# Kernel tuning notes

Measured on AMD Instinct MI355X. Metric: run time of the kernel, lower is better.

Reference implementation:

```python
import jax, jax.numpy as jnp
import numpy as np

S_LEN, B, H, V, L = 128, 128, 1024, 32000, 2
H2 = 512  # ceil(H/2)
WSZ = 10
MAXW = 2 * WSZ + 1


def setup_inputs() -> dict:
    key = jax.random.key(0)
    k = jax.random.split(key, 16)
    def n(ki, shape, s=0.02):
        return jax.random.normal(ki, shape, dtype=jnp.float32) * s
    return {
        "source_sentence_length": S_LEN,
        "encoder_output": jax.random.normal(k[0], (S_LEN, B, H), dtype=jnp.float32),
        "word": jax.random.randint(k[1], (1, B), 0, V),
        "h0": jax.random.normal(k[2], (L, B, H), dtype=jnp.float32),
        "c0": jax.random.normal(k[3], (L, B, H), dtype=jnp.float32),
        "embedding": n(k[4], (V, H)),
        "lstm_Wih": n(k[5], (L, 4 * H, H)),
        "lstm_Whh": n(k[6], (L, 4 * H, H)),
        "lstm_bih": jnp.zeros((L, 4 * H), jnp.float32),
        "lstm_bhh": jnp.zeros((L, 4 * H), jnp.float32),
        "attn_w1": n(k[7], (H2, H)),
        "attn_b1": jnp.zeros((H2,), jnp.float32),
        "attn_w2": n(k[8], (1, H2)),
        "attn_b2": jnp.zeros((1,), jnp.float32),
        "fc1_w": n(k[9], (H, 2 * H)),
        "fc1_b": jnp.zeros((H,), jnp.float32),
        "fc2_w": n(k[10], (V, H)),
        "fc2_b": jnp.zeros((V,), jnp.float32),
    }


def reference(source_sentence_length, encoder_output, word, h0, c0, embedding,
              lstm_Wih, lstm_Whh, lstm_bih, lstm_bhh,
              attn_w1, attn_b1, attn_w2, attn_b2,
              fc1_w, fc1_b, fc2_w, fc2_b):
    S = source_sentence_length
    std2 = (WSZ / 2.0) ** 2  # std_squared from the module

    # embedding lookup: word [1,B] -> [1,B,H]; single-step multi-layer LSTM
    x = embedding[word][0]  # [B,H]
    hs, cs = [], []
    for l in range(h0.shape[0]):
        gates = x @ lstm_Wih[l].T + lstm_bih[l] + h0[l] @ lstm_Whh[l].T + lstm_bhh[l]
        i, f, g, o = jnp.split(gates, 4, axis=-1)
        c = jax.nn.sigmoid(f) * c0[l] + jax.nn.sigmoid(i) * jnp.tanh(g)
        h = jax.nn.sigmoid(o) * jnp.tanh(c)
        hs.append(h); cs.append(c); x = h
    h_new = jnp.stack(hs)
    c_new = jnp.stack(cs)
    out = x[None]  # decoder output [1,B,H]

    # predicted window center p in [0,S]
    p = S * jax.nn.sigmoid(jnp.tanh(out @ attn_w1.T + attn_b1) @ attn_w2.T + attn_b2)
    pb = p[0, :, 0]  # [B]
    ws = jnp.round(jnp.clip(pb - WSZ, 0, None)).astype(jnp.int32)
    we = jnp.round(jnp.clip(pb + WSZ, None, S - 1)).astype(jnp.int32)

    # windowed gather: position j of window b is source index ws[b]+j
    idx = ws[:, None] + jnp.arange(MAXW, dtype=jnp.int32)  # [B,MAXW]
    valid = idx <= we[:, None]
    enc_b = encoder_output.transpose(1, 0, 2)  # [B,S,H]
    h_s = jnp.take_along_axis(enc_b, jnp.clip(idx, 0, S - 1)[:, :, None], axis=1)
    h_s = jnp.where(valid[:, :, None], h_s, 0.0)  # zero-padded as in the torch code

    # faithful (non-negative, non-squared) gaussian term: exp((pos - p)/(2*std^2))
    gauss = jnp.where(valid, jnp.exp((idx.astype(enc_b.dtype) - pb[:, None]) / (2.0 * std2)), 0.0)

    scores = jnp.einsum('bh,bwh->bw', out[0], h_s)  # zero-padded slots score 0, kept in softmax
    a = jax.nn.softmax(scores, axis=-1) * gauss  # [B,MAXW]
    ctx = jnp.einsum('bw,bwh->bh', a, h_s)[None]  # [1,B,H]

    cat = jnp.concatenate([ctx, out], axis=2)  # [1,B,2H]
    o2 = jnp.tanh(cat @ fc1_w.T + fc1_b)
    y = jax.nn.log_softmax(o2 @ fc2_w.T + fc2_b, axis=2)  # [1,B,V]
    return (y, o2, h_new, c_new, a)
```

## Files before the change

kernel.cpp:

```cpp
#include <hip/hip_runtime.h>
#include <math.h>

namespace {

constexpr int B    = 128;
constexpr int H    = 1024;
constexpr int V    = 32000;
constexpr int WSZ  = 10;
constexpr int MAXW = 2 * WSZ + 1;

typedef __attribute__((ext_vector_type(8))) short bf16x8;
typedef __attribute__((ext_vector_type(4))) short short4v;
typedef __attribute__((ext_vector_type(4))) float f32x4;

__device__ __forceinline__ float sigf(float x) { return 1.0f / (1.0f + expf(-x)); }

__device__ __forceinline__ unsigned short rnebf(float f) {
    unsigned u = __float_as_uint(f);
    u += 0x7fffu + ((u >> 16) & 1u);
    return (unsigned short)(u >> 16);
}

__device__ __forceinline__ bf16x8 cvt8(const f32x4 a, const f32x4 b) {
    bf16x8 r;
    r[0] = (short)rnebf(a.x); r[1] = (short)rnebf(a.y);
    r[2] = (short)rnebf(a.z); r[3] = (short)rnebf(a.w);
    r[4] = (short)rnebf(b.x); r[5] = (short)rnebf(b.y);
    r[6] = (short)rnebf(b.z); r[7] = (short)rnebf(b.w);
    return r;
}

__device__ __forceinline__ void gl_lds16(const float* g, float* l) {
    __builtin_amdgcn_global_load_lds(
        (const __attribute__((address_space(1))) unsigned int*)g,
        (__attribute__((address_space(3))) unsigned int*)l,
        16, 0, 0);
}

struct S3 { short h, m, l; };

__device__ __forceinline__ S3 split3(float x) {
    S3 r;
    const unsigned uh = __float_as_uint(x) & 0xFFFF0000u;
    const float fh = __uint_as_float(uh);
    const float r1 = x - fh;
    const unsigned um = __float_as_uint(r1) & 0xFFFF0000u;
    const float fm = __uint_as_float(um);
    const float r2 = r1 - fm;
    const unsigned ul = __float_as_uint(r2) & 0xFFFF0000u;
    r.h = (short)(uh >> 16);
    r.m = (short)(um >> 16);
    r.l = (short)(ul >> 16);
    return r;
}

__device__ __forceinline__ void split8(const f32x4 a, const f32x4 b,
                                       bf16x8& wh, bf16x8& wm, bf16x8& wl) {
    S3 s;
    s = split3(a.x); wh[0] = s.h; wm[0] = s.m; wl[0] = s.l;
    s = split3(a.y); wh[1] = s.h; wm[1] = s.m; wl[1] = s.l;
    s = split3(a.z); wh[2] = s.h; wm[2] = s.m; wl[2] = s.l;
    s = split3(a.w); wh[3] = s.h; wm[3] = s.m; wl[3] = s.l;
    s = split3(b.x); wh[4] = s.h; wm[4] = s.m; wl[4] = s.l;
    s = split3(b.y); wh[5] = s.h; wm[5] = s.m; wl[5] = s.l;
    s = split3(b.z); wh[6] = s.h; wm[6] = s.m; wl[6] = s.l;
    s = split3(b.w); wh[7] = s.h; wm[7] = s.m; wl[7] = s.l;
}

__global__ __launch_bounds__(256, 2) void lstm_gemm(
    const short* __restrict__ Ah0, const short* __restrict__ Am0, const short* __restrict__ Al0,
    const short* __restrict__ Ah1, const short* __restrict__ Am1, const short* __restrict__ Al1,
    const float* __restrict__ W0, const float* __restrict__ W1,
    float* __restrict__ outbase)
{
    __shared__ float wt[2][4160];

    const int t    = threadIdx.x;
    const int lane = t & 63;
    const int w    = t >> 6;
    const int m16  = lane & 15;
    const int g    = lane >> 4;
    const int n0   = blockIdx.x * 64;
    const int y    = blockIdx.y;
    const int src  = y >> 2;
    const int k0   = (y & 3) * 256;
    const short* Ah = src ? Ah1 : Ah0;
    const short* Am = src ? Am1 : Am0;
    const short* Al = src ? Al1 : Al0;
    const float* W  = src ? W1  : W0;
    float* out = outbase + (size_t)y * 128 * 4096;

    bf16x8 ah[2][8], am[2][8], al[2][8];
    #pragma unroll
    for (int q = 0; q < 2; ++q) {
        const size_t ao = (size_t)((w * 2 + q) * 16 + m16) * 1024 + k0 + g * 8;
        #pragma unroll
        for (int s = 0; s < 8; ++s) {
            ah[q][s] = *(const bf16x8*)(Ah + ao + s * 32);
            am[q][s] = *(const bf16x8*)(Am + ao + s * 32);
            al[q][s] = *(const bf16x8*)(Al + ao + s * 32);
        }
    }

#define LSTM_STAGE(BUF, C)                                                  \
    {                                                                       \
        _Pragma("unroll")                                                   \
        for (int i = 0; i < 5; ++i) {                                       \
            const int idx = i * 256 + t;                                    \
            const int rr  = idx / 65;                                       \
            const int pp  = idx - rr * 65;                                  \
            if (idx < 1040 && pp < 64) {                                    \
                const float* s_ = W + (size_t)(n0 + (C) * 16 + rr) * 1024   \
                                + k0 + pp * 4;                              \
                gl_lds16(s_, &wt[BUF][(size_t)(i * 256 + w * 64) * 4]);     \
            }                                                               \
        }                                                                   \
    }

    LSTM_STAGE(0, 0)
    int cur = 0;
    #pragma unroll
    for (int c = 0; c < 4; ++c) {
        __syncthreads();
        if (c < 3) {
            if (cur == 0) LSTM_STAGE(1, c + 1)
            else          LSTM_STAGE(0, c + 1)
        }
        f32x4 acc0 = {}, acc1 = {};
        const float* lrow = &wt[cur][m16 * 260 + g * 8];
        #pragma unroll
        for (int s = 0; s < 8; ++s) {
            const f32x4 wa = *(const f32x4*)(lrow + s * 32);
            const f32x4 wb = *(const f32x4*)(lrow + s * 32 + 4);
            bf16x8 wh, wm, wl;
            split8(wa, wb, wh, wm, wl);
            acc0 = __builtin_amdgcn_mfma_f32_16x16x32_bf16(ah[0][s], wh, acc0, 0, 0, 0);
            acc0 = __builtin_amdgcn_mfma_f32_16x16x32_bf16(ah[0][s], wm, acc0, 0, 0, 0);
            acc0 = __builtin_amdgcn_mfma_f32_16x16x32_bf16(am[0][s], wh, acc0, 0, 0, 0);
            acc0 = __builtin_amdgcn_mfma_f32_16x16x32_bf16(ah[0][s], wl, acc0, 0, 0, 0);
            acc0 = __builtin_amdgcn_mfma_f32_16x16x32_bf16(am[0][s], wm, acc0, 0, 0, 0);
            acc0 = __builtin_amdgcn_mfma_f32_16x16x32_bf16(al[0][s], wh, acc0, 0, 0, 0);
            acc1 = __builtin_amdgcn_mfma_f32_16x16x32_bf16(ah[1][s], wh, acc1, 0, 0, 0);
            acc1 = __builtin_amdgcn_mfma_f32_16x16x32_bf16(ah[1][s], wm, acc1, 0, 0, 0);
            acc1 = __builtin_amdgcn_mfma_f32_16x16x32_bf16(am[1][s], wh, acc1, 0, 0, 0);
            acc1 = __builtin_amdgcn_mfma_f32_16x16x32_bf16(ah[1][s], wl, acc1, 0, 0, 0);
            acc1 = __builtin_amdgcn_mfma_f32_16x16x32_bf16(am[1][s], wm, acc1, 0, 0, 0);
            acc1 = __builtin_amdgcn_mfma_f32_16x16x32_bf16(al[1][s], wh, acc1, 0, 0, 0);
        }
        const int col = n0 + c * 16 + m16;
        #pragma unroll
        for (int j = 0; j < 4; ++j) {
            out[(size_t)(w * 32 + g * 4 + j) * 4096 + col]      = acc0[j];
            out[(size_t)(w * 32 + 16 + g * 4 + j) * 4096 + col] = acc1[j];
        }
        cur ^= 1;
    }
#undef LSTM_STAGE
}

__global__ __launch_bounds__(256, 2) void fc2_gemm(
    const short* __restrict__ A, const float* __restrict__ W,
    const float* __restrict__ bias, float* __restrict__ out)
{
    __shared__ float wt[2][16 * 516];

    const int t    = threadIdx.x;
    const int lane = t & 63;
    const int w    = t >> 6;
    const int m16  = lane & 15;
    const int g    = lane >> 4;
    const int n0   = blockIdx.x * 64;

    bf16x8 a[2][32];
    #pragma unroll
    for (int q = 0; q < 2; ++q) {
        const short* ap = A + (size_t)((w * 2 + q) * 16 + m16) * 1024 + g * 8;
        #pragma unroll
        for (int s = 0; s < 32; ++s)
            a[q][s] = *(const bf16x8*)(ap + s * 32);
    }

#define FC2_STAGE(BUF, C)                                                   \
    {                                                                       \
        _Pragma("unroll")                                                   \
        for (int i = 0; i < 9; ++i) {                                       \
            const int idx = i * 256 + t;                                    \
            const int rr  = idx / 129;                                      \
            const int pp  = idx - rr * 129;                                 \
            if (idx < 2064 && pp < 128) {                                   \
                const float* src = W                                        \
                    + (size_t)(n0 + ((C) >> 1) * 16 + rr) * 1024            \
                    + ((C) & 1) * 512 + pp * 4;                             \
                gl_lds16(src, &wt[BUF][(size_t)(i * 256 + w * 64) * 4]);    \
            }                                                               \
        }                                                                   \
    }

    FC2_STAGE(0, 0)
    int cur = 0;
    f32x4 acc0 = {}, acc1 = {};
    #pragma unroll
    for (int c = 0; c < 8; ++c) {
        __syncthreads();
        if (c < 7) {
            if (cur == 0) FC2_STAGE(1, c + 1)
            else          FC2_STAGE(0, c + 1)
        }
        if ((c & 1) == 0) { acc0 = {}; acc1 = {}; }
        const float* lrow = &wt[cur][m16 * 516 + g * 8];
        #pragma unroll
        for (int s = 0; s < 16; ++s) {
            const f32x4 wa = *(const f32x4*)(lrow + s * 32);
            const f32x4 wb = *(const f32x4*)(lrow + s * 32 + 4);
            const bf16x8 bfr = cvt8(wa, wb);
            const int ks = (c & 1) * 16 + s;
            acc0 = __builtin_amdgcn_mfma_f32_16x16x32_bf16(a[0][ks], bfr, acc0, 0, 0, 0);
            acc1 = __builtin_amdgcn_mfma_f32_16x16x32_bf16(a[1][ks], bfr, acc1, 0, 0, 0);
        }
        if (c & 1) {
            const int col = n0 + (c >> 1) * 16 + m16;
            const float bv = bias[col];
            #pragma unroll
            for (int j = 0; j < 4; ++j) {
                out[(size_t)(w * 32 + g * 4 + j) * V + col]      = acc0[j] + bv;
                out[(size_t)(w * 32 + 16 + g * 4 + j) * V + col] = acc1[j] + bv;
            }
        }
        cur ^= 1;
    }
#undef FC2_STAGE
}

__global__ __launch_bounds__(256, 2) void gemm_x3(
    const short* __restrict__ Ah0, const short* __restrict__ Am0, const short* __restrict__ Al0,
    const short* __restrict__ Ah1, const short* __restrict__ Am1, const short* __restrict__ Al1,
    const float* __restrict__ W0, const float* __restrict__ W1,
    int N, int Ksz, int ks_log2, float* __restrict__ outbase)
{
    const int y = blockIdx.y;
    const int src = y >> ks_log2;
    const short* Ah = src ? Ah1 : Ah0;
    const short* Am = src ? Am1 : Am0;
    const short* Al = src ? Al1 : Al0;
    const float* W  = src ? W1  : W0;
    const int k0 = (y & ((1 << ks_log2) - 1)) * Ksz;
    float* out = outbase + (size_t)y * 128 * N;

    const int t    = threadIdx.x;
    const int lane = t & 63;
    const int wv   = t >> 6;
    const int n0   = blockIdx.x * 64 + wv * 16;
    const int m16  = lane & 15;
    const int ko8  = (lane >> 4) * 8;

    const float* wp = W + (size_t)(n0 + m16) * 1024 + k0 + ko8;
    const size_t a0 = (size_t)m16 * 1024 + k0 + ko8;

    f32x4 acc[8] = {};

    f32x4 cwa = *(const f32x4*)(wp);      f32x4 cwb = *(const f32x4*)(wp + 4);
    f32x4 nwa = *(const f32x4*)(wp + 32); f32x4 nwb = *(const f32x4*)(wp + 36);

    for (int kc = 0; kc + 64 < Ksz; kc += 32) {
        bf16x8 ah[8], am[8], al[8];
        #pragma unroll
        for (int m = 0; m < 8; ++m) {
            const size_t ao = a0 + (size_t)m * 16384 + kc;
            ah[m] = *(const bf16x8*)(Ah + ao);
            am[m] = *(const bf16x8*)(Am + ao);
            al[m] = *(const bf16x8*)(Al + ao);
        }
        __builtin_amdgcn_sched_barrier(0);
        const f32x4 fwa = *(const f32x4*)(wp + kc + 64);
        const f32x4 fwb = *(const f32x4*)(wp + kc + 68);
        bf16x8 wh, wm, wl;
        split8(cwa, cwb, wh, wm, wl);
        #pragma unroll
        for (int m = 0; m < 8; ++m) {
            acc[m] = __builtin_amdgcn_mfma_f32_16x16x32_bf16(ah[m], wh, acc[m], 0, 0, 0);
            acc[m] = __builtin_amdgcn_mfma_f32_16x16x32_bf16(ah[m], wm, acc[m], 0, 0, 0);
            acc[m] = __builtin_amdgcn_mfma_f32_16x16x32_bf16(am[m], wh, acc[m], 0, 0, 0);
            acc[m] = __builtin_amdgcn_mfma_f32_16x16x32_bf16(ah[m], wl, acc[m], 0, 0, 0);
            acc[m] = __builtin_amdgcn_mfma_f32_16x16x32_bf16(am[m], wm, acc[m], 0, 0, 0);
            acc[m] = __builtin_amdgcn_mfma_f32_16x16x32_bf16(al[m], wh, acc[m], 0, 0, 0);
        }
        cwa = nwa; cwb = nwb; nwa = fwa; nwb = fwb;
    }
    #pragma unroll
    for (int tail = 0; tail < 2; ++tail) {
        const int kc = Ksz - 64 + tail * 32;
        bf16x8 ah[8], am[8], al[8];
        #pragma unroll
        for (int m = 0; m < 8; ++m) {
            const size_t ao = a0 + (size_t)m * 16384 + kc;
            ah[m] = *(const bf16x8*)(Ah + ao);
            am[m] = *(const bf16x8*)(Am + ao);
            al[m] = *(const bf16x8*)(Al + ao);
        }
        const f32x4 wa = tail ? nwa : cwa;
        const f32x4 wb = tail ? nwb : cwb;
        bf16x8 wh, wm, wl;
        split8(wa, wb, wh, wm, wl);
        #pragma unroll
        for (int m = 0; m < 8; ++m) {
            acc[m] = __builtin_amdgcn_mfma_f32_16x16x32_bf16(ah[m], wh, acc[m], 0, 0, 0);
            acc[m] = __builtin_amdgcn_mfma_f32_16x16x32_bf16(ah[m], wm, acc[m], 0, 0, 0);
            acc[m] = __builtin_amdgcn_mfma_f32_16x16x32_bf16(am[m], wh, acc[m], 0, 0, 0);
            acc[m] = __builtin_amdgcn_mfma_f32_16x16x32_bf16(ah[m], wl, acc[m], 0, 0, 0);
            acc[m] = __builtin_amdgcn_mfma_f32_16x16x32_bf16(am[m], wm, acc[m], 0, 0, 0);
            acc[m] = __builtin_amdgcn_mfma_f32_16x16x32_bf16(al[m], wh, acc[m], 0, 0, 0);
        }
    }

    #pragma unroll
    for (int m = 0; m < 8; ++m) {
        const int rbase = m * 16 + (lane >> 4) * 4;
        #pragma unroll
        for (int r = 0; r < 4; ++r)
            out[(size_t)(rbase + r) * N + n0 + m16] = acc[m][r];
    }
}

__global__ __launch_bounds__(256, 2) void fc1_gemm(
    const short* __restrict__ A0, const short* __restrict__ A1,
    const float* __restrict__ W, float* __restrict__ outbase)
{
    __shared__ float wt[2][16 * 132];

    const int t    = threadIdx.x;
    const int lane = t & 63;
    const int w    = t >> 6;
    const int m16  = lane & 15;
    const int g    = lane >> 4;
    const int n0   = blockIdx.x * 64;
    const int y    = blockIdx.y;
    const int src  = y >> 3;
    const int k0   = (y & 7) * 128;
    const int wk0  = src * 1024 + k0;
    const short* A = src ? A1 : A0;
    float* out = outbase + (size_t)y * 128 * 1024;

    bf16x8 a[2][4];
    #pragma unroll
    for (int q = 0; q < 2; ++q) {
        const short* ap = A + (size_t)((w * 2 + q) * 16 + m16) * 1024 + k0 + g * 8;
        #pragma unroll
        for (int s = 0; s < 4; ++s)
            a[q][s] = *(const bf16x8*)(ap + s * 32);
    }

#define FC1_STAGE(BUF, C)                                                   \
    {                                                                       \
        _Pragma("unroll")                                                   \
        for (int i = 0; i < 3; ++i) {                                       \
            const int idx = i * 256 + t;                                    \
            const int rr  = idx / 33;                                       \
            const int pp  = idx - rr * 33;                                  \
            if (idx < 528 && pp < 32) {                                     \
                const float* s_ = W + (size_t)(n0 + (C) * 16 + rr) * 2048   \
                                + wk0 + pp * 4;                             \
                gl_lds16(s_, &wt[BUF][(size_t)(i * 256 + w * 64) * 4]);     \
            }                                                               \
        }                                                                   \
    }

    FC1_STAGE(0, 0)
    int cur = 0;
    #pragma unroll
    for (int c = 0; c < 4; ++c) {
        __syncthreads();
        if (c < 3) {
            if (cur == 0) FC1_STAGE(1, c + 1)
            else          FC1_STAGE(0, c + 1)
        }
        f32x4 acc0 = {}, acc1 = {};
        const float* lrow = &wt[cur][m16 * 132 + g * 8];
        #pragma unroll
        for (int s = 0; s < 4; ++s) {
            const f32x4 wa = *(const f32x4*)(lrow + s * 32);
            const f32x4 wb = *(const f32x4*)(lrow + s * 32 + 4);
            const bf16x8 bfr = cvt8(wa, wb);
            acc0 = __builtin_amdgcn_mfma_f32_16x16x32_bf16(a[0][s], bfr, acc0, 0, 0, 0);
            acc1 = __builtin_amdgcn_mfma_f32_16x16x32_bf16(a[1][s], bfr, acc1, 0, 0, 0);
        }
        const int col = n0 + c * 16 + m16;
        #pragma unroll
        for (int j = 0; j < 4; ++j) {
            out[(size_t)(w * 32 + g * 4 + j) * 1024 + col]      = acc0[j];
            out[(size_t)(w * 32 + 16 + g * 4 + j) * 1024 + col] = acc1[j];
        }
        cur ^= 1;
    }
#undef FC1_STAGE
}

__global__ void prep_k(const int* __restrict__ word, const float* __restrict__ emb,
                       const float* __restrict__ h0,
                       short* __restrict__ xh, short* __restrict__ xm, short* __restrict__ xl,
                       short* __restrict__ h0h, short* __restrict__ h0m, short* __restrict__ h0l)
{
    const int blk = blockIdx.x, t = threadIdx.x;
    const float* src; short *dh, *dm, *dl; size_t off;
    if (blk < 128) {
        src = emb + (size_t)word[blk] * H; off = (size_t)blk * H;
        dh = xh; dm = xm; dl = xl;
    } else {
        const int i = blk - 128;
        src = h0 + (size_t)i * H; off = (size_t)i * H;
        dh = h0h; dm = h0m; dl = h0l;
    }
    const float4 v = ((const float4*)src)[t];
    short4v sh, sm, sl;
    S3 s;
    s = split3(v.x); sh.x = s.h; sm.x = s.m; sl.x = s.l;
    s = split3(v.y); sh.y = s.h; sm.y = s.m; sl.y = s.l;
    s = split3(v.z); sh.z = s.h; sm.z = s.m; sl.z = s.l;
    s = split3(v.w); sh.w = s.h; sm.w = s.m; sl.w = s.l;
    *(short4v*)(dh + off + t * 4) = sh;
    *(short4v*)(dm + off + t * 4) = sm;
    *(short4v*)(dl + off + t * 4) = sl;
}

__global__ void lstm_cell_k(const float* __restrict__ part,
                            const float* __restrict__ bih, const float* __restrict__ bhh,
                            const float* __restrict__ c0,
                            float* __restrict__ h_out, float* __restrict__ c_out,
                            short* __restrict__ xh, short* __restrict__ xm,
                            short* __restrict__ xl)
{
    const int idx = blockIdx.x * 256 + threadIdx.x;
    const int b = idx >> 10, hh = idx & 1023;
    const size_t base = (size_t)b * 4096;
    float g[4];
    #pragma unroll
    for (int j = 0; j < 4; ++j) {
        const int o = hh + j * H;
        float s = bih[o] + bhh[o];
        #pragma unroll
        for (int i = 0; i < 8; ++i) s += part[base + o + (size_t)i * 524288];
        g[j] = s;
    }
    const float c = sigf(g[1]) * c0[idx] + sigf(g[0]) * tanhf(g[2]);
    const float h = sigf(g[3]) * tanhf(c);
    c_out[idx] = c;
    h_out[idx] = h;
    const S3 s = split3(h);
    xh[idx] = s.h; xm[idx] = s.m; xl[idx] = s.l;
}

__global__ void attn_ctx_k(const float* __restrict__ part, const float* __restrict__ b1,
                           const float* __restrict__ w2v, const float* __restrict__ b2,
                           const int* __restrict__ Sptr,
                           const float* __restrict__ x, const float* __restrict__ enc,
                           float* __restrict__ a_out, short* __restrict__ ctxb)
{
    __shared__ float red[256];
    __shared__ float so[H];
    __shared__ float swred[4][MAXW];
    __shared__ float ssc[MAXW];
    __shared__ float sa[MAXW];
    __shared__ float sp;
    __shared__ int sw0, sw1;
    const int b = blockIdx.x, t = threadIdx.x;
    const int lane = t & 63, wvv = t >> 6;

    {
        const float* pa = part + (size_t)b * 512;
        float v = 0.f;
        #pragma unroll
        for (int jj = 0; jj < 2; ++jj) {
            const int j = t + jj * 256;
            float sgm = b1[j];
            #pragma unroll
            for (int i = 0; i < 16; ++i) sgm += pa[j + (size_t)i * 65536];
            v += tanhf(sgm) * w2v[j];
        }
        red[t] = v;
        __syncthreads();
        for (int s = 128; s > 0; s >>= 1) {
            if (t < s) red[t] += red[t + s];
            __syncthreads();
        }
        if (t == 0) {
            const float S = (float)Sptr[0];
            const float sv = S * sigf(red[0] + b2[0]);
            sp  = sv;
            sw0 = (int)rintf(fmaxf(sv - (float)WSZ, 0.f));
            sw1 = (int)rintf(fminf(sv + (float)WSZ, S - 1.f));
        }
    }
    for (int h = t; h < H; h += 256) so[h] = x[(size_t)b * H + h];
    __syncthreads();
    const int w0 = sw0, w1e = sw1;
    const float pbv = sp;

    float ps[MAXW];
    #pragma unroll
    for (int w = 0; w < MAXW; ++w) ps[w] = 0.f;
    for (int h4 = t; h4 < H / 4; h4 += 256) {
        const float4 o = ((const float4*)so)[h4];
        #pragma unroll
        for (int w = 0; w < MAXW; ++w) {
            const int idx = w0 + w;
            if (idx <= w1e) {
                const float4 e = *(const float4*)(enc + ((size_t)idx * B + b) * H + h4 * 4);
                ps[w] += o.x * e.x + o.y * e.y + o.z * e.z + o.w * e.w;
            }
        }
    }
    #pragma unroll
    for (int w = 0; w < MAXW; ++w) {
        float v = ps[w];
        for (int off = 32; off > 0; off >>= 1) v += __shfl_down(v, off);
        if (lane == 0) swred[wvv][w] = v;
    }
    __syncthreads();
    if (t == 0) {
        float m = -1e30f;
        for (int w = 0; w < MAXW; ++w) {
            const float s = swred[0][w] + swred[1][w] + swred[2][w] + swred[3][w];
            ssc[w] = s;
            m = fmaxf(m, s);
        }
        float den = 0.f;
        for (int w = 0; w < MAXW; ++w) den += expf(ssc[w] - m);
        for (int w = 0; w < MAXW; ++w) {
            const int idx = w0 + w;
            const float gauss = (idx <= w1e) ? expf(((float)idx - pbv) / 50.0f) : 0.f;
            sa[w] = expf(ssc[w] - m) / den * gauss;
        }
    }
    __syncthreads();
    if (t < MAXW) a_out[b * MAXW + t] = sa[t];
    for (int h4 = t; h4 < H / 4; h4 += 256) {
        float4 acc = {0.f, 0.f, 0.f, 0.f};
        #pragma unroll
        for (int w = 0; w < MAXW; ++w) {
            const int idx = w0 + w;
            if (idx <= w1e) {
                const float4 e = *(const float4*)(enc + ((size_t)idx * B + b) * H + h4 * 4);
                acc.x += sa[w] * e.x; acc.y += sa[w] * e.y;
                acc.z += sa[w] * e.z; acc.w += sa[w] * e.w;
            }
        }
        short4v s;
        s.x = (short)rnebf(acc.x); s.y = (short)rnebf(acc.y);
        s.z = (short)rnebf(acc.z); s.w = (short)rnebf(acc.w);
        *(short4v*)(ctxb + (size_t)b * H + h4 * 4) = s;
    }
}

__global__ void fc1_fin_k(const float* __restrict__ part, const float* __restrict__ bias,
                          float* __restrict__ o2, short* __restrict__ o2b)
{
    const int idx = blockIdx.x * 256 + threadIdx.x;
    const int n = idx & 1023;
    float v = bias[n];
    #pragma unroll
    for (int i = 0; i < 16; ++i) v += part[idx + (size_t)i * 131072];
    v = tanhf(v);
    o2[idx] = v;
    o2b[idx] = (short)rnebf(v);
}

__global__ __launch_bounds__(1024) void lsm_k(float* __restrict__ y)
{
    __shared__ float sm[16], ss[16], slse;
    const int b = blockIdx.x, t = threadIdx.x;
    float* yrow = y + (size_t)b * V;

    f32x4 r[8];
    float m = -1e30f, s = 0.f;
    #pragma unroll
    for (int i = 0; i < 8; ++i) {
        const int v4 = t + i * 1024;
        if (v4 < V / 4) {
            const f32x4 q = ((const f32x4*)yrow)[v4];
            r[i] = q;
            const float mm = fmaxf(fmaxf(q.x, q.y), fmaxf(q.z, q.w));
            if (mm > m) { s *= expf(m - mm); m = mm; }
            s += expf(q.x - m) + expf(q.y - m) + expf(q.z - m) + expf(q.w - m);
        }
    }
    for (int off = 32; off > 0; off >>= 1) {
        const float mo = __shfl_down(m, off), so = __shfl_down(s, off);
        const float mn = fmaxf(m, mo);
        s = s * expf(m - mn) + so * expf(mo - mn);
        m = mn;
    }
    const int wv = t >> 6, lane = t & 63;
    if (lane == 0) { sm[wv] = m; ss[wv] = s; }
    __syncthreads();
    if (t == 0) {
        float M = sm[0], S = ss[0];
        for (int i = 1; i < 16; ++i) {
            const float mn = fmaxf(M, sm[i]);
            S = S * expf(M - mn) + ss[i] * expf(sm[i] - mn);
            M = mn;
        }
        slse = M + logf(S);
    }
    __syncthreads();
    const float lse = slse;
    #pragma unroll
    for (int i = 0; i < 8; ++i) {
        const int v4 = t + i * 1024;
        if (v4 < V / 4) {
            f32x4 q = r[i];
            q.x -= lse; q.y -= lse; q.z -= lse; q.w -= lse;
            ((f32x4*)yrow)[v4] = q;
        }
    }
}

}

extern "C" void kernel_launch(void* const* d_in, const int* in_sizes, int n_in,
                              void* d_out, int out_size, void* d_ws, size_t ws_size,
                              hipStream_t stream)
{
    const int*   Sp   = (const int*)d_in[0];
    const float* enc  = (const float*)d_in[1];
    const int*   word = (const int*)d_in[2];
    const float* h0   = (const float*)d_in[3];
    const float* c0   = (const float*)d_in[4];
    const float* emb  = (const float*)d_in[5];
    const float* Wih  = (const float*)d_in[6];
    const float* Whh  = (const float*)d_in[7];
    const float* bih  = (const float*)d_in[8];
    const float* bhh  = (const float*)d_in[9];
    const float* aw1  = (const float*)d_in[10];
    const float* ab1  = (const float*)d_in[11];
    const float* aw2  = (const float*)d_in[12];
    const float* ab2  = (const float*)d_in[13];
    const float* f1w  = (const float*)d_in[14];
    const float* f1b  = (const float*)d_in[15];
    const float* f2w  = (const float*)d_in[16];
    const float* f2b  = (const float*)d_in[17];

    float* outp = (float*)d_out;
    float* y    = outp;
    float* o2   = y  + (size_t)B * V;
    float* hN   = o2 + (size_t)B * H;
    float* cN   = hN + 2 * (size_t)B * H;
    float* aO   = cN + 2 * (size_t)B * H;

    char* wsp = (char*)d_ws;
    short* xh   = (short*)wsp;  wsp += (size_t)B * H * 2;
    short* xm   = (short*)wsp;  wsp += (size_t)B * H * 2;
    short* xl   = (short*)wsp;  wsp += (size_t)B * H * 2;
    short* h0h  = (short*)wsp;  wsp += (size_t)2 * B * H * 2;
    short* h0m  = (short*)wsp;  wsp += (size_t)2 * B * H * 2;
    short* h0l  = (short*)wsp;  wsp += (size_t)2 * B * H * 2;
    short* ctxb = (short*)wsp;  wsp += (size_t)B * H * 2;
    short* o2b  = (short*)wsp;  wsp += (size_t)B * H * 2;
    float* part = (float*)wsp;  wsp += (size_t)16 * B * 4 * H * 4;

    prep_k<<<dim3(384), dim3(256), 0, stream>>>(word, emb, h0, xh, xm, xl, h0h, h0m, h0l);

    for (int l = 0; l < 2; ++l) {
        lstm_gemm<<<dim3(64, 8), dim3(256), 0, stream>>>(
            xh, xm, xl,
            h0h + (size_t)l * B * H, h0m + (size_t)l * B * H, h0l + (size_t)l * B * H,
            Wih + (size_t)l * 4 * H * H, Whh + (size_t)l * 4 * H * H,
            part);
        lstm_cell_k<<<dim3(B * H / 256), dim3(256), 0, stream>>>(
            part, bih + (size_t)l * 4 * H, bhh + (size_t)l * 4 * H,
            c0 + (size_t)l * B * H,
            hN + (size_t)l * B * H, cN + (size_t)l * B * H, xh, xm, xl);
    }

    const float* hfin = hN + (size_t)B * H;

    gemm_x3<<<dim3(8, 16), dim3(256), 0, stream>>>(
        xh, xm, xl, xh, xm, xl, aw1, aw1, 512, 64, 4, part);
    attn_ctx_k<<<dim3(B), dim3(256), 0, stream>>>(
        part, ab1, aw2, ab2, Sp, hfin, enc, aO, ctxb);

    fc1_gemm<<<dim3(16, 16), dim3(256), 0, stream>>>(ctxb, xh, f1w, part);
    fc1_fin_k<<<dim3(B * H / 256), dim3(256), 0, stream>>>(part, f1b, o2, o2b);

    fc2_gemm<<<dim3(V / 64), dim3(256), 0, stream>>>(o2b, f2w, f2b, y);

    lsm_k<<<dim3(B), dim3(1024), 0, stream>>>(y);
}
```

Measured before the change: 200.5 us.

## Split fc2 GEMM along K into two partials and fold sum plus bias into log-softmax

The fc2 GEMM now runs as a 500x2 grid, each block covering half of K (512), and writes float partial logits to a new workspace buffer. The log-softmax kernel reads both partials plus the bias and sums them before reducing, so the bias add leaves the GEMM epilogue. The K split doubles the block count and halves A-fragment registers per thread, and the 2-blocks-per-CU launch bound is dropped. In exchange an extra B*V*4 bytes of partial output is written and read back, adding memory traffic.

```diff
diff --git a/kernel.cpp b/kernel.cpp
--- a/kernel.cpp
+++ b/kernel.cpp
@@ -158,9 +158,9 @@
 #undef LSTM_STAGE
 }
 
-__global__ __launch_bounds__(256, 2) void fc2_gemm(
+__global__ __launch_bounds__(256) void fc2_gemm(
     const short* __restrict__ A, const float* __restrict__ W,
-    const float* __restrict__ bias, float* __restrict__ out)
+    float* __restrict__ outbase)
 {
     __shared__ float wt[2][16 * 516];
 
@@ -170,13 +170,16 @@
     const int m16  = lane & 15;
     const int g    = lane >> 4;
     const int n0   = blockIdx.x * 64;
-
-    bf16x8 a[2][32];
+    const int y    = blockIdx.y;
+    const int k0   = y * 512;
+    float* out = outbase + (size_t)y * B * V;
+
+    bf16x8 a[2][16];
     #pragma unroll
     for (int q = 0; q < 2; ++q) {
-        const short* ap = A + (size_t)((w * 2 + q) * 16 + m16) * 1024 + g * 8;
-        #pragma unroll
-        for (int s = 0; s < 32; ++s)
+        const short* ap = A + (size_t)((w * 2 + q) * 16 + m16) * 1024 + k0 + g * 8;
+        #pragma unroll
+        for (int s = 0; s < 16; ++s)
             a[q][s] = *(const bf16x8*)(ap + s * 32);
     }
 
@@ -188,9 +191,8 @@
             const int rr  = idx / 129;                                      \
             const int pp  = idx - rr * 129;                                 \
             if (idx < 2064 && pp < 128) {                                   \
-                const float* src = W                                        \
-                    + (size_t)(n0 + ((C) >> 1) * 16 + rr) * 1024            \
-                    + ((C) & 1) * 512 + pp * 4;                             \
+                const float* src = W + (size_t)(n0 + (C) * 16 + rr) * 1024  \
+                                 + k0 + pp * 4;                             \
                 gl_lds16(src, &wt[BUF][(size_t)(i * 256 + w * 64) * 4]);    \
             }                                                               \
         }                                                                   \
@@ -198,33 +200,28 @@
 
     FC2_STAGE(0, 0)
     int cur = 0;
-    f32x4 acc0 = {}, acc1 = {};
-    #pragma unroll
-    for (int c = 0; c < 8; ++c) {
+    #pragma unroll
+    for (int c = 0; c < 4; ++c) {
         __syncthreads();
-        if (c < 7) {
+        if (c < 3) {
             if (cur == 0) FC2_STAGE(1, c + 1)
             else          FC2_STAGE(0, c + 1)
         }
-        if ((c & 1) == 0) { acc0 = {}; acc1 = {}; }
+        f32x4 acc0 = {}, acc1 = {};
         const float* lrow = &wt[cur][m16 * 516 + g * 8];
         #pragma unroll
         for (int s = 0; s < 16; ++s) {
             const f32x4 wa = *(const f32x4*)(lrow + s * 32);
             const f32x4 wb = *(const f32x4*)(lrow + s * 32 + 4);
             const bf16x8 bfr = cvt8(wa, wb);
-            const int ks = (c & 1) * 16 + s;
-            acc0 = __builtin_amdgcn_mfma_f32_16x16x32_bf16(a[0][ks], bfr, acc0, 0, 0, 0);
-            acc1 = __builtin_amdgcn_mfma_f32_16x16x32_bf16(a[1][ks], bfr, acc1, 0, 0, 0);
-        }
-        if (c & 1) {
-            const int col = n0 + (c >> 1) * 16 + m16;
-            const float bv = bias[col];
-            #pragma unroll
-            for (int j = 0; j < 4; ++j) {
-                out[(size_t)(w * 32 + g * 4 + j) * V + col]      = acc0[j] + bv;
-                out[(size_t)(w * 32 + 16 + g * 4 + j) * V + col] = acc1[j] + bv;
-            }
+            acc0 = __builtin_amdgcn_mfma_f32_16x16x32_bf16(a[0][s], bfr, acc0, 0, 0, 0);
+            acc1 = __builtin_amdgcn_mfma_f32_16x16x32_bf16(a[1][s], bfr, acc1, 0, 0, 0);
+        }
+        const int col = n0 + c * 16 + m16;
+        #pragma unroll
+        for (int j = 0; j < 4; ++j) {
+            out[(size_t)(w * 32 + g * 4 + j) * V + col]      = acc0[j];
+            out[(size_t)(w * 32 + 16 + g * 4 + j) * V + col] = acc1[j];
         }
         cur ^= 1;
     }
@@ -563,10 +560,14 @@
     o2b[idx] = (short)rnebf(v);
 }
 
-__global__ __launch_bounds__(1024) void lsm_k(float* __restrict__ y)
+__global__ __launch_bounds__(1024) void lsm_k(
+    const float* __restrict__ p0, const float* __restrict__ p1,
+    const float* __restrict__ bias, float* __restrict__ y)
 {
     __shared__ float sm[16], ss[16], slse;
     const int b = blockIdx.x, t = threadIdx.x;
+    const float* r0 = p0 + (size_t)b * V;
+    const float* r1 = p1 + (size_t)b * V;
     float* yrow = y + (size_t)b * V;
 
     f32x4 r[8];
@@ -575,7 +576,12 @@
     for (int i = 0; i < 8; ++i) {
         const int v4 = t + i * 1024;
         if (v4 < V / 4) {
-            const f32x4 q = ((const f32x4*)yrow)[v4];
+            const f32x4 a = ((const f32x4*)r0)[v4];
+            const f32x4 c = ((const f32x4*)r1)[v4];
+            const f32x4 bv = ((const f32x4*)bias)[v4];
+            f32x4 q;
+            q.x = a.x + c.x + bv.x; q.y = a.y + c.y + bv.y;
+            q.z = a.z + c.z + bv.z; q.w = a.w + c.w + bv.w;
             r[i] = q;
             const float mm = fmaxf(fmaxf(q.x, q.y), fmaxf(q.z, q.w));
             if (mm > m) { s *= expf(m - mm); m = mm; }
@@ -655,6 +661,7 @@
     short* ctxb = (short*)wsp;  wsp += (size_t)B * H * 2;
     short* o2b  = (short*)wsp;  wsp += (size_t)B * H * 2;
     float* part = (float*)wsp;  wsp += (size_t)16 * B * 4 * H * 4;
+    float* pf2  = (float*)wsp;  wsp += (size_t)2 * B * V * 4;
 
     prep_k<<<dim3(384), dim3(256), 0, stream>>>(word, emb, h0, xh, xm, xl, h0h, h0m, h0l);
 
@@ -680,7 +687,7 @@
     fc1_gemm<<<dim3(16, 16), dim3(256), 0, stream>>>(ctxb, xh, f1w, part);
     fc1_fin_k<<<dim3(B * H / 256), dim3(256), 0, stream>>>(part, f1b, o2, o2b);
 
-    fc2_gemm<<<dim3(V / 64), dim3(256), 0, stream>>>(o2b, f2w, f2b, y);
-
-    lsm_k<<<dim3(B), dim3(1024), 0, stream>>>(y);
-}
+    fc2_gemm<<<dim3(V / 64, 2), dim3(256), 0, stream>>>(o2b, f2w, pf2);
+
+    lsm_k<<<dim3(B), dim3(1024), 0, stream>>>(pf2, pf2 + (size_t)B * V, f2b, y);
+}
```

Result: faster. 168.8 us (median of 2 runs) (-15.8%).

## Reorder fc2 GEMM loop to load A in K-halves with persistent accumulators

Applied to the files above, without the earlier changes.

The fc2 GEMM now walks the K dimension in two halves. Each wave loads only half of its A fragments (16 per row tile instead of 32) and accumulates all four 16-column output tiles in registers, writing them out at the end. This cuts the live A register footprint, which is meant to reduce register pressure or spills. It also drops the launch_bounds minimum-blocks hint. In exchange it holds 8 accumulators and reloads A once per K-half, and occupancy may change.

```diff
diff --git a/kernel.cpp b/kernel.cpp
--- a/kernel.cpp
+++ b/kernel.cpp
@@ -158,7 +158,7 @@
 #undef LSTM_STAGE
 }
 
-__global__ __launch_bounds__(256, 2) void fc2_gemm(
+__global__ __launch_bounds__(256) void fc2_gemm(
     const short* __restrict__ A, const float* __restrict__ W,
     const float* __restrict__ bias, float* __restrict__ out)
 {
@@ -171,16 +171,9 @@
     const int g    = lane >> 4;
     const int n0   = blockIdx.x * 64;
 
-    bf16x8 a[2][32];
-    #pragma unroll
-    for (int q = 0; q < 2; ++q) {
-        const short* ap = A + (size_t)((w * 2 + q) * 16 + m16) * 1024 + g * 8;
-        #pragma unroll
-        for (int s = 0; s < 32; ++s)
-            a[q][s] = *(const bf16x8*)(ap + s * 32);
-    }
-
-#define FC2_STAGE(BUF, C)                                                   \
+    f32x4 acc[4][2] = {};
+
+#define FC2_STAGE(BUF, KH, C)                                               \
     {                                                                       \
         _Pragma("unroll")                                                   \
         for (int i = 0; i < 9; ++i) {                                       \
@@ -188,47 +181,60 @@
             const int rr  = idx / 129;                                      \
             const int pp  = idx - rr * 129;                                 \
             if (idx < 2064 && pp < 128) {                                   \
-                const float* src = W                                        \
-                    + (size_t)(n0 + ((C) >> 1) * 16 + rr) * 1024            \
-                    + ((C) & 1) * 512 + pp * 4;                             \
+                const float* src = W + (size_t)(n0 + (C) * 16 + rr) * 1024  \
+                                 + (KH) * 512 + pp * 4;                     \
                 gl_lds16(src, &wt[BUF][(size_t)(i * 256 + w * 64) * 4]);    \
             }                                                               \
         }                                                                   \
     }
 
-    FC2_STAGE(0, 0)
+    FC2_STAGE(0, 0, 0)
     int cur = 0;
-    f32x4 acc0 = {}, acc1 = {};
-    #pragma unroll
-    for (int c = 0; c < 8; ++c) {
-        __syncthreads();
-        if (c < 7) {
-            if (cur == 0) FC2_STAGE(1, c + 1)
-            else          FC2_STAGE(0, c + 1)
-        }
-        if ((c & 1) == 0) { acc0 = {}; acc1 = {}; }
-        const float* lrow = &wt[cur][m16 * 516 + g * 8];
-        #pragma unroll
-        for (int s = 0; s < 16; ++s) {
-            const f32x4 wa = *(const f32x4*)(lrow + s * 32);
-            const f32x4 wb = *(const f32x4*)(lrow + s * 32 + 4);
-            const bf16x8 bfr = cvt8(wa, wb);
-            const int ks = (c & 1) * 16 + s;
-            acc0 = __builtin_amdgcn_mfma_f32_16x16x32_bf16(a[0][ks], bfr, acc0, 0, 0, 0);
-            acc1 = __builtin_amdgcn_mfma_f32_16x16x32_bf16(a[1][ks], bfr, acc1, 0, 0, 0);
-        }
-        if (c & 1) {
-            const int col = n0 + (c >> 1) * 16 + m16;
-            const float bv = bias[col];
+    #pragma unroll
+    for (int kh = 0; kh < 2; ++kh) {
+        bf16x8 a[2][16];
+        #pragma unroll
+        for (int q = 0; q < 2; ++q) {
+            const short* ap = A + (size_t)((w * 2 + q) * 16 + m16) * 1024
+                            + kh * 512 + g * 8;
             #pragma unroll
-            for (int j = 0; j < 4; ++j) {
-                out[(size_t)(w * 32 + g * 4 + j) * V + col]      = acc0[j] + bv;
-                out[(size_t)(w * 32 + 16 + g * 4 + j) * V + col] = acc1[j] + bv;
+            for (int s = 0; s < 16; ++s)
+                a[q][s] = *(const bf16x8*)(ap + s * 32);
+        }
+        #pragma unroll
+        for (int c = 0; c < 4; ++c) {
+            __syncthreads();
+            if (c < 3) {
+                if (cur == 0) FC2_STAGE(1, kh, c + 1)
+                else          FC2_STAGE(0, kh, c + 1)
+            } else if (kh == 0) {
+                if (cur == 0) FC2_STAGE(1, 1, 0)
+                else          FC2_STAGE(0, 1, 0)
             }
-        }
-        cur ^= 1;
+            const float* lrow = &wt[cur][m16 * 516 + g * 8];
+            #pragma unroll
+            for (int s = 0; s < 16; ++s) {
+                const f32x4 wa = *(const f32x4*)(lrow + s * 32);
+                const f32x4 wb = *(const f32x4*)(lrow + s * 32 + 4);
+                const bf16x8 bfr = cvt8(wa, wb);
+                acc[c][0] = __builtin_amdgcn_mfma_f32_16x16x32_bf16(a[0][s], bfr, acc[c][0], 0, 0, 0);
+                acc[c][1] = __builtin_amdgcn_mfma_f32_16x16x32_bf16(a[1][s], bfr, acc[c][1], 0, 0, 0);
+            }
+            cur ^= 1;
+        }
     }
 #undef FC2_STAGE
+
+    #pragma unroll
+    for (int c = 0; c < 4; ++c) {
+        const int col = n0 + c * 16 + m16;
+        const float bv = bias[col];
+        #pragma unroll
+        for (int j = 0; j < 4; ++j) {
+            out[(size_t)(w * 32 + g * 4 + j) * V + col]      = acc[c][0][j] + bv;
+            out[(size_t)(w * 32 + 16 + g * 4 + j) * V + col] = acc[c][1][j] + bv;
+        }
+    }
 }
 
 __global__ __launch_bounds__(256, 2) void gemm_x3(
```

Measured after the change: 172.1 us. -14.2%, faster.
